# Kernel tuning notes

Hardware: AMD Instinct MI355X
Metric: run time of the kernel (lower is better)

## Reference

```python
import math
import jax, jax.numpy as jnp
import numpy as np

G_RATIO = 0.5  # g_ratio
TB = 0.001     # tie-break factor in heuristic


def _expand(x, kern):
    # x: [B,H,W]; 3x3 all-ones-except-center neighbor sum (same filter for every sample,
    # so the torch grouped conv is equivalent to a single-channel conv)
    return jax.lax.conv_general_dilated(x[:, None], kern, (1, 1), 'SAME')[:, 0]


def _st_softmax_noexp(val):
    # straight-through soft argmax over flattened map
    B = val.shape[0]
    v = val.reshape(B, -1)
    y = v / v.sum(-1, keepdims=True)
    ind = jnp.argmax(y, axis=-1)
    y_hard = jnp.zeros_like(y).at[jnp.arange(B), ind].set(1.0)
    out = jax.lax.stop_gradient(y_hard - y) + y
    return out.reshape(val.shape)


def _heuristic_dist(goal):
    # chebyshev + TB * euclidean distance to goal; goal: [B,H,W] one-hot
    B, H, W = goal.shape
    loc = jnp.stack(jnp.meshgrid(jnp.arange(H), jnp.arange(W), indexing='ij'), 0).astype(goal.dtype)  # [2,H,W]
    goal_loc = jnp.einsum('kij,bij->bk', loc, goal)              # [B,2]
    diff = loc.reshape(2, -1)[None] - goal_loc[:, :, None]       # [B,2,HW]
    d = jnp.abs(diff)
    h = d.sum(1) - d.min(1)                                      # chebyshev
    euc = jnp.sqrt((diff ** 2).sum(1))
    return (h + TB * euc).reshape(B, H, W)


def _astar(cost_maps, start_maps, goal_maps, heuristic_maps, obstacles_maps):
    cost = cost_maps[:, 0]
    start = start_maps[:, 0]
    goal = goal_maps[:, 0]
    obst = obstacles_maps[:, 0]
    B, H, W = start.shape
    N = H * W
    dt = cost.dtype

    kern = jnp.zeros((1, 1, 3, 3), dt).at[0, 0].set(1.0).at[0, 0, 1, 1].set(0.0)
    h = _heuristic_dist(goal)            # h_choice='dist'
    delta_g = cost                        # g_choice='net-output'
    goal_idx = jnp.argmax(goal.reshape(B, -1), axis=-1)
    parents0 = jnp.ones((B, N), dt) * goal_idx[:, None].astype(dt)
    inv_sqrt = 1.0 / math.sqrt(W)

    def step(carry, t):
        open_m, hist, g, parents, t_fin, done = carry
        f = G_RATIO * g + (1.0 - G_RATIO) * h
        f_exp = jnp.exp(-f * inv_sqrt) * open_m
        sel = _st_softmax_noexp(f_exp)
        dist_to_goal = (sel * goal).sum((1, 2), keepdims=True)
        is_unsolved = (dist_to_goal < 1e-8).astype(dt)

        hist_n = jnp.clip(hist + sel, 0.0, 1.0)
        open_n = jnp.clip(open_m - is_unsolved * sel, 0.0, 1.0)

        nbr = _expand(sel, kern) * obst
        g2 = _expand((g + delta_g) * sel, kern)
        idx = ((1.0 - open_n) * (1.0 - hist_n) + open_n * (g > g2).astype(dt)) * nbr
        idx = jax.lax.stop_gradient(idx)
        g_n = jax.lax.stop_gradient(g2 * idx + g * (1.0 - idx))
        open_n = jax.lax.stop_gradient(jnp.clip(open_n + idx, 0.0, 1.0))

        idx_f = idx.reshape(B, -1)
        new_par = jnp.argmax(sel.reshape(B, -1), axis=-1)[:, None].astype(dt)
        par_n = new_par * idx_f + parents * (1.0 - idx_f)

        # emulate torch's early break: freeze state once all samples are solved
        keep = done
        carry_n = (
            jnp.where(keep, open_m, open_n),
            jnp.where(keep, hist, hist_n),
            jnp.where(keep, g, g_n),
            jnp.where(keep, parents, par_n),
            jnp.where(keep, t_fin, t),
            done | jnp.all(is_unsolved == 0),
        )
        return carry_n, None

    init = (start, jnp.zeros_like(start), jnp.zeros_like(start), parents0,
            jnp.int32(0), jnp.array(False))
    (open_m, hist, g, parents, t_fin, done), _ = jax.lax.scan(
        step, init, jnp.arange(N, dtype=jnp.int32))
    return hist, parents, t_fin


def _backtrack(start, goal, parents_f, t_fin):
    # start/goal: [B,H,W]; parents_f: [B,N] float; t_fin: traced int
    B = start.shape[0]
    parents = parents_f.astype(jnp.int32)
    goal_f = goal.reshape(B, -1).astype(jnp.int32)
    loc0 = (parents * goal_f).sum(-1)

    def body(i, c):
        path, loc = c
        path = path.at[jnp.arange(B), loc].set(1)
        loc = parents[jnp.arange(B), loc]
        return (path, loc)

    path, _ = jax.lax.fori_loop(0, t_fin, body, (goal_f, loc0))
    return path.reshape(start.shape)


def setup_inputs() -> dict:
    key = jax.random.key(0)
    k1, k2, k3, k4 = jax.random.split(key, 4)
    B, H, W = 16, 32, 32
    N = H * W
    cost_maps = jax.random.uniform(k1, (B, 1, H, W), jnp.float32, 0.1, 1.0)
    si = jax.random.randint(k2, (B,), 0, N)
    gi = jax.random.randint(k3, (B,), 0, N)
    gi = jnp.where(gi == si, (gi + 1) % N, gi)
    start_maps = jnp.zeros((B, N), jnp.float32).at[jnp.arange(B), si].set(1.0).reshape(B, 1, H, W)
    goal_maps = jnp.zeros((B, N), jnp.float32).at[jnp.arange(B), gi].set(1.0).reshape(B, 1, H, W)
    heuristic_maps = jax.random.normal(k4, (B, 1, H, W), jnp.float32)
    obstacles_maps = jnp.ones((B, 1, H, W), jnp.float32)
    return {
        'cost_maps': cost_maps,
        'start_maps': start_maps,
        'goal_maps': goal_maps,
        'heuristic_maps': heuristic_maps,
        'obstacles_maps': obstacles_maps,
    }


def reference(cost_maps, start_maps, goal_maps, heuristic_maps, obstacles_maps):
    hist, parents, t_fin = _astar(cost_maps, start_maps, goal_maps, heuristic_maps, obstacles_maps)
    path = _backtrack(start_maps[:, 0], goal_maps[:, 0], parents, t_fin)
    return hist[:, None], path[:, None].astype(cost_maps.dtype)
```

## Files before the change

### kernel.cpp

```cpp
#include <hip/hip_runtime.h>

#define NCELL 1024
#define BATCH 16

__global__ __launch_bounds__(64) void astar_main(
    const float* __restrict__ cost_g,
    const float* __restrict__ start_g,
    const float* __restrict__ goal_g,
    const float* __restrict__ obst_g,
    float* __restrict__ out,
    int* __restrict__ meta,
    unsigned short* __restrict__ wpar)
{
    const int b = blockIdx.x;
    const int lane = threadIdx.x;
    const int base = b * NCELL;
    const float inv = 0.17677669529663687f;

    __shared__ float s_fexp[NCELL];
    __shared__ float s_g[NCELL];
    __shared__ float s_cost[NCELL];
    __shared__ float s_h[NCELL];
    __shared__ unsigned char s_open[NCELL];
    __shared__ unsigned char s_hist[NCELL];
    __shared__ unsigned char s_obst[NCELL];
    __shared__ unsigned short s_par[NCELL];
    __shared__ int s_goal;

    for (int c = lane; c < NCELL; c += 64)
        if (goal_g[base + c] != 0.0f) s_goal = c;
    __syncthreads();
    const int goalidx = s_goal;
    const float gyf = (float)(goalidx >> 5);
    const float gxf = (float)(goalidx & 31);

    for (int c = lane; c < NCELL; c += 64) {
        float costv  = cost_g[base + c];
        float startv = start_g[base + c];
        s_cost[c] = costv;
        s_open[c] = (startv != 0.0f) ? 1 : 0;
        s_hist[c] = 0;
        s_obst[c] = (obst_g[base + c] != 0.0f) ? 1 : 0;
        s_g[c]    = 0.0f;
        s_par[c]  = (unsigned short)goalidx;
        float dy = fabsf((float)(c >> 5) - gyf);
        float dx = fabsf((float)(c & 31) - gxf);
        float hb  = __fsub_rn(__fadd_rn(dy, dx), fminf(dy, dx));
        float euc = sqrtf(__fadd_rn(__fmul_rn(dy, dy), __fmul_rn(dx, dx)));
        float h   = __fadd_rn(hb, __fmul_rn(0.001f, euc));
        s_h[c] = h;
        float f = __fadd_rn(__fmul_rn(0.5f, 0.0f), __fmul_rn(0.5f, h));
        float e = expf(__fmul_rn(-f, inv));
        s_fexp[c] = (startv != 0.0f) ? e : 0.0f;
    }
    __syncthreads();

    int sb = NCELL - 1;
    const int c0 = lane << 4;
    for (int t = 0; t < NCELL; ++t) {
        float v[16];
        ((float4*)v)[0] = ((const float4*)(s_fexp + c0))[0];
        ((float4*)v)[1] = ((const float4*)(s_fexp + c0))[1];
        ((float4*)v)[2] = ((const float4*)(s_fexp + c0))[2];
        ((float4*)v)[3] = ((const float4*)(s_fexp + c0))[3];
        float bv = v[0]; int bi = 0;
        #pragma unroll
        for (int i = 1; i < 16; ++i)
            if (v[i] > bv) { bv = v[i]; bi = i; }
        unsigned long long key =
            (((unsigned long long)__float_as_uint(bv)) << 10) |
            (unsigned long long)(1023 - (c0 + bi));
        #pragma unroll
        for (int m = 1; m < 64; m <<= 1) {
            unsigned long long ok = __shfl_xor(key, m, 64);
            if (ok > key) key = ok;
        }
        const int sel = 1023 - (int)(key & 1023ull);
        const bool solved = (sel == goalidx);

        const float g2v = __fadd_rn(s_g[sel], s_cost[sel]);

        if (lane == 0) {
            s_hist[sel] = 1;
            if (!solved) { s_open[sel] = 0; s_fexp[sel] = 0.0f; }
        }
        if (lane < 9 && lane != 4) {
            const int dr = lane / 3 - 1, dc = lane % 3 - 1;
            const int nr = (sel >> 5) + dr, nc = (sel & 31) + dc;
            if (nr >= 0 && nr < 32 && nc >= 0 && nc < 32) {
                const int p = (nr << 5) + nc;
                const bool o  = s_open[p] != 0;
                const bool hs = s_hist[p] != 0;
                if (s_obst[p] && ((!o && !hs) || (o && (s_g[p] > g2v)))) {
                    s_g[p]   = g2v;
                    s_par[p] = (unsigned short)sel;
                    s_open[p] = 1;
                    float f = __fadd_rn(__fmul_rn(0.5f, g2v),
                                        __fmul_rn(0.5f, s_h[p]));
                    s_fexp[p] = expf(__fmul_rn(-f, inv));
                }
            }
        }
        if (solved) { sb = t; break; }
    }

    for (int c = lane; c < NCELL; c += 64) {
        out[base + c] = s_hist[c] ? 1.0f : 0.0f;
        wpar[base + c] = s_par[c];
    }
    if (lane == 0) { meta[b] = sb; meta[BATCH + b] = goalidx; }
}

__global__ __launch_bounds__(64) void astar_bt(
    const int* __restrict__ meta,
    const unsigned short* __restrict__ wpar,
    float* __restrict__ out)
{
    const int b = blockIdx.x;
    const int lane = threadIdx.x;
    __shared__ unsigned short lpar[NCELL];
    __shared__ unsigned int pmask[32];

    for (int c = lane; c < NCELL; c += 64)
        lpar[c] = wpar[b * NCELL + c];
    if (lane < 32) pmask[lane] = 0u;
    int T = 0;
    #pragma unroll
    for (int i = 0; i < BATCH; ++i) {
        int s = meta[i];
        T = (s > T) ? s : T;
    }
    const int goalidx = meta[BATCH + b];
    __syncthreads();

    if (lane == 0) {
        pmask[goalidx >> 5] |= (1u << (goalidx & 31));
        int loc = lpar[goalidx];
        for (int it = 0; it < T; ++it) {
            unsigned int w   = pmask[loc >> 5];
            unsigned int bit = 1u << (loc & 31);
            if (w & bit) break;
            pmask[loc >> 5] = w | bit;
            loc = lpar[loc];
        }
    }
    __syncthreads();

    for (int c = lane; c < NCELL; c += 64)
        out[BATCH * NCELL + b * NCELL + c] =
            ((pmask[c >> 5] >> (c & 31)) & 1u) ? 1.0f : 0.0f;
}

extern "C" void kernel_launch(void* const* d_in, const int* in_sizes, int n_in,
                              void* d_out, int out_size, void* d_ws, size_t ws_size,
                              hipStream_t stream)
{
    const float* cost  = (const float*)d_in[0];
    const float* start = (const float*)d_in[1];
    const float* goal  = (const float*)d_in[2];
    const float* obst  = (const float*)d_in[4];
    float* out = (float*)d_out;

    int* meta = (int*)d_ws;
    unsigned short* wpar = (unsigned short*)((char*)d_ws + 256);

    astar_main<<<BATCH, 64, 0, stream>>>(cost, start, goal, obst, out, meta, wpar);
    astar_bt<<<BATCH, 64, 0, stream>>>(meta, wpar, out);
}
```

Measured before the change: 88.77 us.

## Fuse backtrack into main A* kernel and use DPP float-max argmax reduction

Merges the backtracking kernel into the search kernel so the parent array stays in LDS and a second launch plus global round trip is avoided. Replaces the 64-bit shuffle-based argmax with a tree-reduced local argmax, a DPP float max reduction, and a ballot to find the lowest winning lane. Also packs open, history and obstacle flags into one word and stores g and cost together as float2. Backtracking now runs up to NCELL steps per sample instead of the batch-wide max step count, which relies on cycle detection to stop early.

```diff
diff --git a/kernel.cpp b/kernel.cpp
--- a/kernel.cpp
+++ b/kernel.cpp
@@ -3,28 +3,31 @@
 #define NCELL 1024
 #define BATCH 16
 
-__global__ __launch_bounds__(64) void astar_main(
+template <int CTRL>
+__device__ __forceinline__ float dppmaxf(float v) {
+    int r = __builtin_amdgcn_update_dpp(__float_as_int(v), __float_as_int(v),
+                                        CTRL, 0xF, 0xF, false);
+    return fmaxf(v, __int_as_float(r));
+}
+
+__global__ __launch_bounds__(64) void astar_fused(
     const float* __restrict__ cost_g,
     const float* __restrict__ start_g,
     const float* __restrict__ goal_g,
     const float* __restrict__ obst_g,
-    float* __restrict__ out,
-    int* __restrict__ meta,
-    unsigned short* __restrict__ wpar)
+    float* __restrict__ out)
 {
     const int b = blockIdx.x;
     const int lane = threadIdx.x;
     const int base = b * NCELL;
     const float inv = 0.17677669529663687f;
 
-    __shared__ float s_fexp[NCELL];
-    __shared__ float s_g[NCELL];
-    __shared__ float s_cost[NCELL];
-    __shared__ float s_h[NCELL];
-    __shared__ unsigned char s_open[NCELL];
-    __shared__ unsigned char s_hist[NCELL];
-    __shared__ unsigned char s_obst[NCELL];
+    __shared__ float  s_fexp[NCELL];
+    __shared__ float2 s_gc[NCELL];
+    __shared__ float  s_h[NCELL];
+    __shared__ unsigned int s_flags[NCELL];
     __shared__ unsigned short s_par[NCELL];
+    __shared__ unsigned int pmask[32];
     __shared__ int s_goal;
 
     for (int c = lane; c < NCELL; c += 64)
@@ -37,25 +40,24 @@
     for (int c = lane; c < NCELL; c += 64) {
         float costv  = cost_g[base + c];
         float startv = start_g[base + c];
-        s_cost[c] = costv;
-        s_open[c] = (startv != 0.0f) ? 1 : 0;
-        s_hist[c] = 0;
-        s_obst[c] = (obst_g[base + c] != 0.0f) ? 1 : 0;
-        s_g[c]    = 0.0f;
-        s_par[c]  = (unsigned short)goalidx;
+        unsigned int fl = 0;
+        if (startv != 0.0f)          fl |= 1u;
+        if (obst_g[base + c] != 0.0f) fl |= 4u;
+        s_flags[c] = fl;
+        s_gc[c] = make_float2(0.0f, costv);
+        s_par[c] = (unsigned short)goalidx;
         float dy = fabsf((float)(c >> 5) - gyf);
         float dx = fabsf((float)(c & 31) - gxf);
         float hb  = __fsub_rn(__fadd_rn(dy, dx), fminf(dy, dx));
         float euc = sqrtf(__fadd_rn(__fmul_rn(dy, dy), __fmul_rn(dx, dx)));
         float h   = __fadd_rn(hb, __fmul_rn(0.001f, euc));
         s_h[c] = h;
-        float f = __fadd_rn(__fmul_rn(0.5f, 0.0f), __fmul_rn(0.5f, h));
+        float f = __fmul_rn(0.5f, h);
         float e = expf(__fmul_rn(-f, inv));
         s_fexp[c] = (startv != 0.0f) ? e : 0.0f;
     }
     __syncthreads();
 
-    int sb = NCELL - 1;
     const int c0 = lane << 4;
     for (int t = 0; t < NCELL; ++t) {
         float v[16];
@@ -63,92 +65,92 @@
         ((float4*)v)[1] = ((const float4*)(s_fexp + c0))[1];
         ((float4*)v)[2] = ((const float4*)(s_fexp + c0))[2];
         ((float4*)v)[3] = ((const float4*)(s_fexp + c0))[3];
-        float bv = v[0]; int bi = 0;
+        float m[8]; int j[8];
         #pragma unroll
-        for (int i = 1; i < 16; ++i)
-            if (v[i] > bv) { bv = v[i]; bi = i; }
-        unsigned long long key =
-            (((unsigned long long)__float_as_uint(bv)) << 10) |
-            (unsigned long long)(1023 - (c0 + bi));
+        for (int i = 0; i < 8; ++i) {
+            bool r = v[2*i+1] > v[2*i];
+            m[i] = r ? v[2*i+1] : v[2*i];
+            j[i] = r ? 2*i+1 : 2*i;
+        }
         #pragma unroll
-        for (int m = 1; m < 64; m <<= 1) {
-            unsigned long long ok = __shfl_xor(key, m, 64);
-            if (ok > key) key = ok;
+        for (int i = 0; i < 4; ++i) {
+            bool r = m[2*i+1] > m[2*i];
+            m[i] = r ? m[2*i+1] : m[2*i];
+            j[i] = r ? j[2*i+1] : j[2*i];
         }
-        const int sel = 1023 - (int)(key & 1023ull);
+        #pragma unroll
+        for (int i = 0; i < 2; ++i) {
+            bool r = m[2*i+1] > m[2*i];
+            m[i] = r ? m[2*i+1] : m[2*i];
+            j[i] = r ? j[2*i+1] : j[2*i];
+        }
+        bool rr = m[1] > m[0];
+        float bv = rr ? m[1] : m[0];
+        int   bi = rr ? j[1] : j[0];
+
+        float w = bv;
+        w = dppmaxf<0x111>(w);
+        w = dppmaxf<0x112>(w);
+        w = dppmaxf<0x114>(w);
+        w = dppmaxf<0x118>(w);
+        w = dppmaxf<0x142>(w);
+        w = dppmaxf<0x143>(w);
+        float vmax = __int_as_float(
+            __builtin_amdgcn_readlane(__float_as_int(w), 63));
+        unsigned long long msk = __ballot(bv == vmax);
+        int winner = (int)__builtin_ctzll(msk);
+        int sel = __builtin_amdgcn_readlane(c0 + bi, winner);
         const bool solved = (sel == goalidx);
 
-        const float g2v = __fadd_rn(s_g[sel], s_cost[sel]);
+        float2 gc = s_gc[sel];
+        const float g2v = __fadd_rn(gc.x, gc.y);
 
-        if (lane == 0) {
-            s_hist[sel] = 1;
-            if (!solved) { s_open[sel] = 0; s_fexp[sel] = 0.0f; }
+        if (lane == 9) {
+            unsigned int fl = s_flags[sel];
+            fl |= 2u;
+            if (!solved) { fl &= ~1u; s_fexp[sel] = 0.0f; }
+            s_flags[sel] = fl;
         }
         if (lane < 9 && lane != 4) {
             const int dr = lane / 3 - 1, dc = lane % 3 - 1;
             const int nr = (sel >> 5) + dr, nc = (sel & 31) + dc;
             if (nr >= 0 && nr < 32 && nc >= 0 && nc < 32) {
                 const int p = (nr << 5) + nc;
-                const bool o  = s_open[p] != 0;
-                const bool hs = s_hist[p] != 0;
-                if (s_obst[p] && ((!o && !hs) || (o && (s_g[p] > g2v)))) {
-                    s_g[p]   = g2v;
+                unsigned int fl = s_flags[p];
+                float gp = s_gc[p].x;
+                bool o  = (fl & 1u) != 0;
+                bool hs = (fl & 2u) != 0;
+                if ((fl & 4u) && ((!o && !hs) || (o && gp > g2v))) {
+                    s_gc[p].x = g2v;
                     s_par[p] = (unsigned short)sel;
-                    s_open[p] = 1;
+                    s_flags[p] = fl | 1u;
                     float f = __fadd_rn(__fmul_rn(0.5f, g2v),
                                         __fmul_rn(0.5f, s_h[p]));
                     s_fexp[p] = expf(__fmul_rn(-f, inv));
                 }
             }
         }
-        if (solved) { sb = t; break; }
+        if (solved) break;
+    }
+
+    if (lane < 32) pmask[lane] = 0u;
+    if (lane == 0) {
+        pmask[goalidx >> 5] |= 1u << (goalidx & 31);
+        int loc = s_par[goalidx];
+        for (int it = 0; it < NCELL; ++it) {
+            unsigned int wd  = pmask[loc >> 5];
+            unsigned int bit = 1u << (loc & 31);
+            if (wd & bit) break;
+            pmask[loc >> 5] = wd | bit;
+            loc = s_par[loc];
+        }
     }
 
     for (int c = lane; c < NCELL; c += 64) {
-        out[base + c] = s_hist[c] ? 1.0f : 0.0f;
-        wpar[base + c] = s_par[c];
+        out[base + c] = (s_flags[c] & 2u) ? 1.0f : 0.0f;
+        out[BATCH * NCELL + base + c] =
+            ((pmask[c >> 5] >> (c & 31)) & 1u) ? 1.0f : 0.0f;
     }
-    if (lane == 0) { meta[b] = sb; meta[BATCH + b] = goalidx; }
-}
-
-__global__ __launch_bounds__(64) void astar_bt(
-    const int* __restrict__ meta,
-    const unsigned short* __restrict__ wpar,
-    float* __restrict__ out)
-{
-    const int b = blockIdx.x;
-    const int lane = threadIdx.x;
-    __shared__ unsigned short lpar[NCELL];
-    __shared__ unsigned int pmask[32];
-
-    for (int c = lane; c < NCELL; c += 64)
-        lpar[c] = wpar[b * NCELL + c];
-    if (lane < 32) pmask[lane] = 0u;
-    int T = 0;
-    #pragma unroll
-    for (int i = 0; i < BATCH; ++i) {
-        int s = meta[i];
-        T = (s > T) ? s : T;
-    }
-    const int goalidx = meta[BATCH + b];
-    __syncthreads();
-
-    if (lane == 0) {
-        pmask[goalidx >> 5] |= (1u << (goalidx & 31));
-        int loc = lpar[goalidx];
-        for (int it = 0; it < T; ++it) {
-            unsigned int w   = pmask[loc >> 5];
-            unsigned int bit = 1u << (loc & 31);
-            if (w & bit) break;
-            pmask[loc >> 5] = w | bit;
-            loc = lpar[loc];
-        }
-    }
-    __syncthreads();
-
-    for (int c = lane; c < NCELL; c += 64)
-        out[BATCH * NCELL + b * NCELL + c] =
-            ((pmask[c >> 5] >> (c & 31)) & 1u) ? 1.0f : 0.0f;
 }
 
 extern "C" void kernel_launch(void* const* d_in, const int* in_sizes, int n_in,
@@ -161,9 +163,5 @@
     const float* obst  = (const float*)d_in[4];
     float* out = (float*)d_out;
 
-    int* meta = (int*)d_ws;
-    unsigned short* wpar = (unsigned short*)((char*)d_ws + 256);
-
-    astar_main<<<BATCH, 64, 0, stream>>>(cost, start, goal, obst, out, meta, wpar);
-    astar_bt<<<BATCH, 64, 0, stream>>>(meta, wpar, out);
+    astar_fused<<<BATCH, 64, 0, stream>>>(cost, start, goal, obst, out);
 }
```

Result: faster. 86.60 us (-2.4%).
